# Optimization experiments

Measured on AMD Instinct MI355X. Metric: run time of the kernel, lower is better.

## Reference

```python
import jax, jax.numpy as jnp
import numpy as np

D_MODEL = 1024
H = 16
D_HEAD = D_MODEL // H
EPS = 1e-5  # torch LayerNorm default


def setup_inputs() -> dict:
    key = jax.random.key(0)
    ks = jax.random.split(key, 10)
    bs, seq = 4, 2048
    scale = 1.0 / np.sqrt(D_MODEL)
    return {
        "q": jax.random.normal(ks[0], (bs, seq, D_MODEL), jnp.float32),
        "k": jax.random.normal(ks[1], (bs, seq, D_MODEL), jnp.float32),
        "v": jax.random.normal(ks[2], (bs, seq, D_MODEL), jnp.float32),
        "zero_mask": jnp.zeros((bs, 1, 1, seq), jnp.float32),
        "Wq": jax.random.normal(ks[3], (D_MODEL, D_MODEL), jnp.float32) * scale,
        "Wk": jax.random.normal(ks[4], (D_MODEL, D_MODEL), jnp.float32) * scale,
        "Wv": jax.random.normal(ks[5], (D_MODEL, D_MODEL), jnp.float32) * scale,
        "Wo": jax.random.normal(ks[6], (D_MODEL, D_MODEL), jnp.float32) * scale,
        "gamma": jnp.ones((D_MODEL,), jnp.float32),
        "beta": jnp.zeros((D_MODEL,), jnp.float32),
    }


def reference(q, k, v, zero_mask, Wq, Wk, Wv, Wo, gamma, beta):
    bs, seq_q, _ = q.shape
    seq_k = k.shape[1]
    residual = q
    # Projections (torch Linear: x @ W.T), split into heads -> (bs, h, seq, d)
    qh = (q @ Wq.T).reshape(bs, seq_q, H, D_HEAD).transpose(0, 2, 1, 3)
    kh = (k @ Wk.T).reshape(bs, seq_k, H, D_HEAD).transpose(0, 2, 1, 3)
    vh = (v @ Wv.T).reshape(bs, seq_k, H, D_HEAD).transpose(0, 2, 1, 3)
    # Scaled dot-product attention with additive -1e9 * zero_mask
    att = jnp.einsum("bhqd,bhkd->bhqk", qh, kh) / np.sqrt(D_HEAD)
    att = att + zero_mask * -1e9
    att = jax.nn.softmax(att, axis=-1)
    # dropout: identity in eval-mode reference
    ctx = jnp.einsum("bhqk,bhkd->bhqd", att, vh)
    ctx = ctx.transpose(0, 2, 1, 3).reshape(bs, seq_q, D_MODEL)
    out = ctx @ Wo.T
    out = out + residual
    # LayerNorm over last dim
    mu = jnp.mean(out, axis=-1, keepdims=True)
    var = jnp.var(out, axis=-1, keepdims=True)
    out = (out - mu) * jax.lax.rsqrt(var + EPS) * gamma + beta
    return out
```

## Files before the change

kernel.cpp:

```cpp
#include <hip/hip_runtime.h>
#include <hip/hip_bf16.h>

typedef __bf16 bf16x8 __attribute__((ext_vector_type(8)));
typedef float  f32x4  __attribute__((ext_vector_type(4)));
typedef short  s16x4  __attribute__((ext_vector_type(4)));

#define D_MODEL 1024
#define SEQ 2048
#define BS 4
#define NH 16
#define DH 64
#define MTOT (BS * SEQ)

#define AS1 __attribute__((address_space(1)))
#define AS3 __attribute__((address_space(3)))

template <typename T>
__device__ inline bf16x8 ld8(const T* p);

template <>
__device__ inline bf16x8 ld8<float>(const float* p) {
    f32x4 a = *(const f32x4*)p;
    f32x4 b = *(const f32x4*)(p + 4);
    bf16x8 r;
    r[0] = (__bf16)a[0]; r[1] = (__bf16)a[1]; r[2] = (__bf16)a[2]; r[3] = (__bf16)a[3];
    r[4] = (__bf16)b[0]; r[5] = (__bf16)b[1]; r[6] = (__bf16)b[2]; r[7] = (__bf16)b[3];
    return r;
}

template <>
__device__ inline bf16x8 ld8<__bf16>(const __bf16* p) {
    return *(const bf16x8*)p;
}

__global__ __launch_bounds__(256) void cvt4_kernel(
    const float* __restrict__ a, const float* __restrict__ b,
    const float* __restrict__ c, const float* __restrict__ e,
    __bf16* __restrict__ x, __bf16* __restrict__ y,
    __bf16* __restrict__ z, __bf16* __restrict__ w)
{
    const float* s = (blockIdx.y == 0) ? a : (blockIdx.y == 1) ? b : (blockIdx.y == 2) ? c : e;
    __bf16*      d = (blockIdx.y == 0) ? x : (blockIdx.y == 1) ? y : (blockIdx.y == 2) ? z : w;
    const long i = ((long)blockIdx.x * 256 + threadIdx.x) * 8;
    *(bf16x8*)(d + i) = ld8<float>(s + i);
}

__global__ __launch_bounds__(256) void gemm_qkv(
    const float* __restrict__ q, const float* __restrict__ k, const float* __restrict__ v,
    const __bf16* __restrict__ Wb,
    __bf16* __restrict__ Qp, __bf16* __restrict__ Kp, __bf16* __restrict__ Vp)
{
    __shared__ __align__(16) __bf16 As[2 * 4096];
    __shared__ __align__(16) __bf16 Bs[2 * 4096];
    const int K = D_MODEL, N = D_MODEL;
    const int z = blockIdx.z;
    const float* A = (z == 0) ? q : (z == 1) ? k : v;
    const __bf16* B = Wb + (long)z * D_MODEL * D_MODEL;
    __bf16* C = (z == 0) ? Qp : (z == 1) ? Kp : Vp;

    const int t = threadIdx.x;
    const int wave = t >> 6, lane = t & 63;
    const int quad = lane >> 4, l15 = lane & 15;
    const int wm = (wave >> 1) * 64, wn = (wave & 1) * 64;
    const long m0 = (long)blockIdx.x * 128;
    const long n0 = (long)blockIdx.y * 128;
    const int sr = t >> 2, sc = (t & 3) * 8;

    const __bf16* gB = B + (n0 + sr) * (long)K + sc;
    __bf16* lB0 = Bs + wave * 512;
    __bf16* lB1 = Bs + 2048 + wave * 512;
    __bf16* lB2 = Bs + 4096 + wave * 512;
    __bf16* lB3 = Bs + 6144 + wave * 512;

    f32x4 acc[4][4] = {};

    for (int k0 = 0; k0 < K; k0 += 64) {
        __builtin_amdgcn_global_load_lds((const AS1 void*)(gB + k0),               (AS3 void*)lB0, 16, 0, 0);
        __builtin_amdgcn_global_load_lds((const AS1 void*)(gB + 64 * K + k0),      (AS3 void*)lB1, 16, 0, 0);
        __builtin_amdgcn_global_load_lds((const AS1 void*)(gB + k0 + 32),          (AS3 void*)lB2, 16, 0, 0);
        __builtin_amdgcn_global_load_lds((const AS1 void*)(gB + 64 * K + k0 + 32), (AS3 void*)lB3, 16, 0, 0);
        *(bf16x8*)&As[sr * 32 + sc]               = ld8<float>(&A[(m0 + sr) * K + k0 + sc]);
        *(bf16x8*)&As[(sr + 64) * 32 + sc]        = ld8<float>(&A[(m0 + sr + 64) * K + k0 + sc]);
        *(bf16x8*)&As[4096 + sr * 32 + sc]        = ld8<float>(&A[(m0 + sr) * K + k0 + 32 + sc]);
        *(bf16x8*)&As[4096 + (sr + 64) * 32 + sc] = ld8<float>(&A[(m0 + sr + 64) * K + k0 + 32 + sc]);
        __syncthreads();
#pragma unroll
        for (int p = 0; p < 2; ++p) {
            bf16x8 af[4], bfr[4];
#pragma unroll
            for (int i = 0; i < 4; ++i) af[i]  = *(const bf16x8*)&As[p * 4096 + (wm + i * 16 + l15) * 32 + quad * 8];
#pragma unroll
            for (int i = 0; i < 4; ++i) bfr[i] = *(const bf16x8*)&Bs[p * 4096 + (wn + i * 16 + l15) * 32 + quad * 8];
#pragma unroll
            for (int i = 0; i < 4; ++i)
#pragma unroll
                for (int j = 0; j < 4; ++j)
                    acc[i][j] = __builtin_amdgcn_mfma_f32_16x16x32_bf16(af[i], bfr[j], acc[i][j], 0, 0, 0);
        }
        __syncthreads();
    }

#pragma unroll
    for (int i = 0; i < 4; ++i)
#pragma unroll
        for (int j = 0; j < 4; ++j) {
            const long r = m0 + wm + i * 16 + quad * 4;
            const long c = n0 + wn + j * 16 + l15;
#pragma unroll
            for (int reg = 0; reg < 4; ++reg)
                C[(r + reg) * N + c] = (__bf16)acc[i][j][reg];
        }
}

__global__ __launch_bounds__(256) void gemm_bb(
    const __bf16* __restrict__ A, const __bf16* __restrict__ B,
    __bf16* __restrict__ C, int M, int N, int K)
{
    __shared__ __align__(16) __bf16 As[2 * 4096];
    __shared__ __align__(16) __bf16 Bs[2 * 4096];
    const int t = threadIdx.x;
    const int wave = t >> 6, lane = t & 63;
    const int quad = lane >> 4, l15 = lane & 15;
    const int wm = (wave >> 1) * 64, wn = (wave & 1) * 64;
    const long m0 = (long)blockIdx.x * 128;
    const long n0 = (long)blockIdx.y * 128;
    const int sr = t >> 2, sc = (t & 3) * 8;

    const __bf16* gA = A + (m0 + sr) * (long)K + sc;
    const __bf16* gB = B + (n0 + sr) * (long)K + sc;
    __bf16* lA0 = As + wave * 512;
    __bf16* lA1 = As + 2048 + wave * 512;
    __bf16* lA2 = As + 4096 + wave * 512;
    __bf16* lA3 = As + 6144 + wave * 512;
    __bf16* lB0 = Bs + wave * 512;
    __bf16* lB1 = Bs + 2048 + wave * 512;
    __bf16* lB2 = Bs + 4096 + wave * 512;
    __bf16* lB3 = Bs + 6144 + wave * 512;

    f32x4 acc[4][4] = {};

    for (int k0 = 0; k0 < K; k0 += 64) {
        __builtin_amdgcn_global_load_lds((const AS1 void*)(gA + k0),               (AS3 void*)lA0, 16, 0, 0);
        __builtin_amdgcn_global_load_lds((const AS1 void*)(gA + 64 * K + k0),      (AS3 void*)lA1, 16, 0, 0);
        __builtin_amdgcn_global_load_lds((const AS1 void*)(gA + k0 + 32),          (AS3 void*)lA2, 16, 0, 0);
        __builtin_amdgcn_global_load_lds((const AS1 void*)(gA + 64 * K + k0 + 32), (AS3 void*)lA3, 16, 0, 0);
        __builtin_amdgcn_global_load_lds((const AS1 void*)(gB + k0),               (AS3 void*)lB0, 16, 0, 0);
        __builtin_amdgcn_global_load_lds((const AS1 void*)(gB + 64 * K + k0),      (AS3 void*)lB1, 16, 0, 0);
        __builtin_amdgcn_global_load_lds((const AS1 void*)(gB + k0 + 32),          (AS3 void*)lB2, 16, 0, 0);
        __builtin_amdgcn_global_load_lds((const AS1 void*)(gB + 64 * K + k0 + 32), (AS3 void*)lB3, 16, 0, 0);
        __syncthreads();
#pragma unroll
        for (int p = 0; p < 2; ++p) {
            bf16x8 af[4], bfr[4];
#pragma unroll
            for (int i = 0; i < 4; ++i) af[i]  = *(const bf16x8*)&As[p * 4096 + (wm + i * 16 + l15) * 32 + quad * 8];
#pragma unroll
            for (int i = 0; i < 4; ++i) bfr[i] = *(const bf16x8*)&Bs[p * 4096 + (wn + i * 16 + l15) * 32 + quad * 8];
#pragma unroll
            for (int i = 0; i < 4; ++i)
#pragma unroll
                for (int j = 0; j < 4; ++j)
                    acc[i][j] = __builtin_amdgcn_mfma_f32_16x16x32_bf16(af[i], bfr[j], acc[i][j], 0, 0, 0);
        }
        __syncthreads();
    }

#pragma unroll
    for (int i = 0; i < 4; ++i)
#pragma unroll
        for (int j = 0; j < 4; ++j) {
            const long r = m0 + wm + i * 16 + quad * 4;
            const long c = n0 + wn + j * 16 + l15;
#pragma unroll
            for (int reg = 0; reg < 4; ++reg)
                C[(r + reg) * N + c] = (__bf16)acc[i][j][reg];
        }
}

__global__ __launch_bounds__(256) void attn_kernel(
    const __bf16* Qp, const __bf16* __restrict__ Kp, const __bf16* __restrict__ Vp,
    const float* __restrict__ mask, __bf16* Ctx)
{
    __shared__ __align__(16) __bf16 Ks[64][72];
    __shared__ __align__(16) __bf16 Vt[64][76];
    __shared__ __align__(16) float  Ms[64];

    const int t = threadIdx.x;
    const int wave = t >> 6, lane = t & 63;
    const int quad = lane >> 4, l15 = lane & 15;
    const int qt = blockIdx.x;
    const int bh = blockIdx.y;
    const int b = bh >> 4, h = bh & 15;
    const long rowbase = (long)b * SEQ;
    const int q0 = qt * 128 + wave * 16;

    bf16x8 aq[2][2];
#pragma unroll
    for (int qi = 0; qi < 2; ++qi) {
        const long qrow = rowbase + q0 + qi * 64 + l15;
        const __bf16* qptr = Qp + qrow * D_MODEL + h * DH + quad * 8;
        aq[qi][0] = *(const bf16x8*)(qptr);
        aq[qi][1] = *(const bf16x8*)(qptr + 32);
    }

    const s16x4 ones = {(short)0x3F80, (short)0x3F80, (short)0x3F80, (short)0x3F80};

    f32x4 acc_l[2] = {};
    f32x4 acc_o[2][4] = {};

    const int sr = t >> 2, sc = (t & 3) * 16;
    const int kp2 = (t >> 3) * 2, dc = (t & 7) * 8;
    const float C1 = 0.125f * 1.44269504f;
    const float C2 = -1e9f * 1.44269504f;

    for (int kt = 0; kt < SEQ / 64; ++kt) {
        __syncthreads();
        {
            const __bf16* kptr = Kp + (rowbase + kt * 64 + sr) * D_MODEL + h * DH + sc;
            *(bf16x8*)&Ks[sr][sc]     = *(const bf16x8*)(kptr);
            *(bf16x8*)&Ks[sr][sc + 8] = *(const bf16x8*)(kptr + 8);
            const __bf16* vptr = Vp + (rowbase + kt * 64 + kp2) * D_MODEL + h * DH + dc;
            bf16x8 v0 = *(const bf16x8*)(vptr);
            bf16x8 v1 = *(const bf16x8*)(vptr + D_MODEL);
#pragma unroll
            for (int e = 0; e < 8; ++e) {
                union { __bf16 h2[2]; unsigned u; } pk;
                pk.h2[0] = v0[e]; pk.h2[1] = v1[e];
                *(unsigned*)&Vt[dc + e][kp2] = pk.u;
            }
            if (t < 64) Ms[t] = mask[rowbase + kt * 64 + t] * C2;
        }
        __syncthreads();

        bf16x8 kf[4][2];
#pragma unroll
        for (int nt = 0; nt < 4; ++nt)
#pragma unroll
            for (int ks = 0; ks < 2; ++ks)
                kf[nt][ks] = *(const bf16x8*)&Ks[nt * 16 + l15][ks * 32 + quad * 8];
        s16x4 vtf[4][4];
#pragma unroll
        for (int nt = 0; nt < 4; ++nt)
#pragma unroll
            for (int dt = 0; dt < 4; ++dt)
                vtf[nt][dt] = *(const s16x4*)&Vt[dt * 16 + l15][nt * 16 + quad * 4];
        f32x4 mv[4];
#pragma unroll
        for (int nt = 0; nt < 4; ++nt)
            mv[nt] = *(const f32x4*)&Ms[nt * 16 + quad * 4];

#pragma unroll
        for (int qi = 0; qi < 2; ++qi) {
            f32x4 st[4] = {};
#pragma unroll
            for (int ks = 0; ks < 2; ++ks)
#pragma unroll
                for (int nt = 0; nt < 4; ++nt)
                    st[nt] = __builtin_amdgcn_mfma_f32_16x16x32_bf16(kf[nt][ks], aq[qi][ks], st[nt], 0, 0, 0);
            s16x4 pp[4];
#pragma unroll
            for (int nt = 0; nt < 4; ++nt) {
                float pv0 = __builtin_amdgcn_exp2f(fmaf(st[nt][0], C1, mv[nt][0]));
                float pv1 = __builtin_amdgcn_exp2f(fmaf(st[nt][1], C1, mv[nt][1]));
                float pv2 = __builtin_amdgcn_exp2f(fmaf(st[nt][2], C1, mv[nt][2]));
                float pv3 = __builtin_amdgcn_exp2f(fmaf(st[nt][3], C1, mv[nt][3]));
                union { __hip_bfloat162 h2[2]; s16x4 s; } u;
                u.h2[0] = __float22bfloat162_rn(float2{pv0, pv1});
                u.h2[1] = __float22bfloat162_rn(float2{pv2, pv3});
                pp[nt] = u.s;
            }
#pragma unroll
            for (int nt = 0; nt < 4; ++nt) {
#pragma unroll
                for (int dt = 0; dt < 4; ++dt)
                    acc_o[qi][dt] = __builtin_amdgcn_mfma_f32_16x16x16bf16_1k(pp[nt], vtf[nt][dt], acc_o[qi][dt], 0, 0, 0);
                acc_l[qi] = __builtin_amdgcn_mfma_f32_16x16x16bf16_1k(pp[nt], ones, acc_l[qi], 0, 0, 0);
            }
        }
    }

#pragma unroll
    for (int qi = 0; qi < 2; ++qi)
#pragma unroll
        for (int reg = 0; reg < 4; ++reg) {
            const float inv = 1.f / acc_l[qi][reg];
            const long row = rowbase + q0 + qi * 64 + quad * 4 + reg;
#pragma unroll
            for (int dt = 0; dt < 4; ++dt)
                Ctx[row * D_MODEL + h * DH + dt * 16 + l15] = (__bf16)(acc_o[qi][dt][reg] * inv);
        }
}

__global__ __launch_bounds__(256) void ln_kernel(
    const __bf16* __restrict__ Y, const float* __restrict__ R,
    const float* __restrict__ gamma, const float* __restrict__ beta,
    float* __restrict__ Out)
{
    __shared__ float red[8];
    const long row = blockIdx.x;
    const int t = threadIdx.x;
    const int wave = t >> 6, lane = t & 63;
    float x[4];
    float s = 0.f, s2 = 0.f;
#pragma unroll
    for (int i = 0; i < 4; ++i) {
        const int idx = i * 256 + t;
        const float v = (float)Y[row * D_MODEL + idx] + R[row * D_MODEL + idx];
        x[i] = v; s += v; s2 += v * v;
    }
#pragma unroll
    for (int off = 32; off >= 1; off >>= 1) {
        s  += __shfl_xor(s, off, 64);
        s2 += __shfl_xor(s2, off, 64);
    }
    if (lane == 0) { red[wave] = s; red[4 + wave] = s2; }
    __syncthreads();
    s  = red[0] + red[1] + red[2] + red[3];
    s2 = red[4] + red[5] + red[6] + red[7];
    const float mu   = s * (1.f / 1024.f);
    const float var  = s2 * (1.f / 1024.f) - mu * mu;
    const float rstd = rsqrtf(var + 1e-5f);
#pragma unroll
    for (int i = 0; i < 4; ++i) {
        const int idx = i * 256 + t;
        Out[row * D_MODEL + idx] = (x[i] - mu) * rstd * gamma[idx] + beta[idx];
    }
}

extern "C" void kernel_launch(void* const* d_in, const int* in_sizes, int n_in,
                              void* d_out, int out_size, void* d_ws, size_t ws_size,
                              hipStream_t stream)
{
    const float* q     = (const float*)d_in[0];
    const float* k     = (const float*)d_in[1];
    const float* v     = (const float*)d_in[2];
    const float* mask  = (const float*)d_in[3];
    const float* Wq    = (const float*)d_in[4];
    const float* Wk    = (const float*)d_in[5];
    const float* Wv    = (const float*)d_in[6];
    const float* Wo    = (const float*)d_in[7];
    const float* gamma = (const float*)d_in[8];
    const float* beta  = (const float*)d_in[9];
    float* out = (float*)d_out;

    const long NACT = (long)MTOT * D_MODEL;
    const long NW   = (long)D_MODEL * D_MODEL;

    __bf16* Qp = (__bf16*)d_ws;
    __bf16* Kp = Qp + NACT;
    __bf16* Vp = (__bf16*)d_out;
    __bf16* Wb = Vp + NACT;
    __bf16 *Wqb = Wb, *Wkb = Wb + NW, *Wvb = Wb + 2 * NW, *Wob = Wb + 3 * NW;
    __bf16* Y = Kp;

    cvt4_kernel<<<dim3(NW / 2048, 4), 256, 0, stream>>>(Wq, Wk, Wv, Wo, Wqb, Wkb, Wvb, Wob);

    gemm_qkv<<<dim3(MTOT / 128, D_MODEL / 128, 3), 256, 0, stream>>>(q, k, v, Wqb, Qp, Kp, Vp);

    attn_kernel<<<dim3(SEQ / 128, BS * NH), 256, 0, stream>>>(Qp, Kp, Vp, mask, Qp);

    gemm_bb<<<dim3(MTOT / 128, D_MODEL / 128), 256, 0, stream>>>(Qp, Wob, Y, MTOT, D_MODEL, D_MODEL);

    ln_kernel<<<MTOT, 256, 0, stream>>>(Y, q, gamma, beta, out);
}
```

Baseline: 390.1 us.

## Double-buffer K/V/mask tiles in attention with register prefetch of next tile

The attention kernel now keeps two LDS buffers for K, transposed V and mask, and loads the next key tile from global memory into registers while the current tile is being computed. This drops one __syncthreads per iteration and hides global load latency behind the MFMA work. In exchange it doubles LDS use per block, which may lower occupancy, and adds register pressure from the prefetched values.

```diff
diff --git a/kernel.cpp b/kernel.cpp
--- a/kernel.cpp
+++ b/kernel.cpp
@@ -181,9 +181,9 @@
     const __bf16* Qp, const __bf16* __restrict__ Kp, const __bf16* __restrict__ Vp,
     const float* __restrict__ mask, __bf16* Ctx)
 {
-    __shared__ __align__(16) __bf16 Ks[64][72];
-    __shared__ __align__(16) __bf16 Vt[64][76];
-    __shared__ __align__(16) float  Ms[64];
+    __shared__ __align__(16) __bf16 Ks[2][64][72];
+    __shared__ __align__(16) __bf16 Vt[2][64][76];
+    __shared__ __align__(16) float  Ms[2][64];
 
     const int t = threadIdx.x;
     const int wave = t >> 6, lane = t & 63;
@@ -213,41 +213,54 @@
     const float C1 = 0.125f * 1.44269504f;
     const float C2 = -1e9f * 1.44269504f;
 
+    const __bf16* kbase = Kp + (rowbase + sr) * D_MODEL + h * DH + sc;
+    const __bf16* vbase = Vp + (rowbase + kp2) * D_MODEL + h * DH + dc;
+
+    bf16x8 kr0 = *(const bf16x8*)(kbase);
+    bf16x8 kr1 = *(const bf16x8*)(kbase + 8);
+    bf16x8 vr0 = *(const bf16x8*)(vbase);
+    bf16x8 vr1 = *(const bf16x8*)(vbase + D_MODEL);
+    float  mreg = (t < 64) ? mask[rowbase + t] * C2 : 0.f;
+
     for (int kt = 0; kt < SEQ / 64; ++kt) {
-        __syncthreads();
+        const int buf = kt & 1;
+        *(bf16x8*)&Ks[buf][sr][sc]     = kr0;
+        *(bf16x8*)&Ks[buf][sr][sc + 8] = kr1;
+#pragma unroll
+        for (int e = 0; e < 8; ++e) {
+            union { __bf16 h2[2]; unsigned u; } pk;
+            pk.h2[0] = vr0[e]; pk.h2[1] = vr1[e];
+            *(unsigned*)&Vt[buf][dc + e][kp2] = pk.u;
+        }
+        if (t < 64) Ms[buf][t] = mreg;
+        __syncthreads();
+
         {
-            const __bf16* kptr = Kp + (rowbase + kt * 64 + sr) * D_MODEL + h * DH + sc;
-            *(bf16x8*)&Ks[sr][sc]     = *(const bf16x8*)(kptr);
-            *(bf16x8*)&Ks[sr][sc + 8] = *(const bf16x8*)(kptr + 8);
-            const __bf16* vptr = Vp + (rowbase + kt * 64 + kp2) * D_MODEL + h * DH + dc;
-            bf16x8 v0 = *(const bf16x8*)(vptr);
-            bf16x8 v1 = *(const bf16x8*)(vptr + D_MODEL);
-#pragma unroll
-            for (int e = 0; e < 8; ++e) {
-                union { __bf16 h2[2]; unsigned u; } pk;
-                pk.h2[0] = v0[e]; pk.h2[1] = v1[e];
-                *(unsigned*)&Vt[dc + e][kp2] = pk.u;
-            }
-            if (t < 64) Ms[t] = mask[rowbase + kt * 64 + t] * C2;
-        }
-        __syncthreads();
+            const int ktn = (kt + 1 < SEQ / 64) ? kt + 1 : kt;
+            const long off = (long)ktn * 64 * D_MODEL;
+            kr0 = *(const bf16x8*)(kbase + off);
+            kr1 = *(const bf16x8*)(kbase + off + 8);
+            vr0 = *(const bf16x8*)(vbase + off);
+            vr1 = *(const bf16x8*)(vbase + off + D_MODEL);
+            mreg = (t < 64) ? mask[rowbase + ktn * 64 + t] * C2 : 0.f;
+        }
 
         bf16x8 kf[4][2];
 #pragma unroll
         for (int nt = 0; nt < 4; ++nt)
 #pragma unroll
             for (int ks = 0; ks < 2; ++ks)
-                kf[nt][ks] = *(const bf16x8*)&Ks[nt * 16 + l15][ks * 32 + quad * 8];
+                kf[nt][ks] = *(const bf16x8*)&Ks[buf][nt * 16 + l15][ks * 32 + quad * 8];
         s16x4 vtf[4][4];
 #pragma unroll
         for (int nt = 0; nt < 4; ++nt)
 #pragma unroll
             for (int dt = 0; dt < 4; ++dt)
-                vtf[nt][dt] = *(const s16x4*)&Vt[dt * 16 + l15][nt * 16 + quad * 4];
+                vtf[nt][dt] = *(const s16x4*)&Vt[buf][dt * 16 + l15][nt * 16 + quad * 4];
         f32x4 mv[4];
 #pragma unroll
         for (int nt = 0; nt < 4; ++nt)
-            mv[nt] = *(const f32x4*)&Ms[nt * 16 + quad * 4];
+            mv[nt] = *(const f32x4*)&Ms[buf][nt * 16 + quad * 4];
 
 #pragma unroll
         for (int qi = 0; qi < 2; ++qi) {
```

Result: faster. 366.2 us (-6.1%).
